# Kernel optimization log

Measured on AMD Instinct MI355X. Metric: run time of the kernel, lower is better.

Reference implementation:

```python
import jax, jax.numpy as jnp
import numpy as np

B, S, D, H = 1, 2048, 1024, 16
HD = D // H  # head_dim = 64


def _split_heads(x):
    # [B,S,D] -> [B,H,S,HD]
    return x.reshape(B, S, H, HD).transpose(0, 2, 1, 3)


def setup_inputs() -> dict:
    key = jax.random.key(0)
    ks = jax.random.split(key, 8)
    p = 0.02
    return {
        "hidden_states": jax.random.normal(ks[0], (B, S, D), jnp.float32),
        "knowledge": jax.random.normal(ks[1], (B, S, D), jnp.float32),
        "Wq": jax.random.normal(ks[2], (2 * D, D), jnp.float32) * p,
        "Wk_know": jax.random.normal(ks[3], (D, D), jnp.float32) * p,
        "Wk_mlp": jax.random.normal(ks[4], (D, D), jnp.float32) * p,
        "Wv_know": jax.random.normal(ks[5], (D, D), jnp.float32) * p,
        "Wv_mlp": jax.random.normal(ks[6], (D, D), jnp.float32) * p,
        "Wo": jax.random.normal(ks[7], (D, D), jnp.float32) * p,
    }


def reference(hidden_states, knowledge, Wq, Wk_know, Wk_mlp, Wv_know, Wv_mlp, Wo):
    shared = jnp.concatenate([hidden_states, knowledge], axis=-1)  # [B,S,2D]
    q = _split_heads(shared @ Wq)            # [B,H,S,HD]
    k_know = _split_heads(knowledge @ Wk_know)
    k_mlp = _split_heads(hidden_states @ Wk_mlp)
    v_know = _split_heads(knowledge @ Wv_know)
    v_mlp = _split_heads(hidden_states @ Wv_mlp)

    scale = jnp.asarray(D, jnp.float32) ** 0.5  # note: full embed_dim, not head_dim
    mask_value = jnp.finfo(jnp.float32).min
    causal = jnp.tril(jnp.ones((S, S), dtype=bool))  # [S,S]

    s_know = jnp.einsum("bhqd,bhkd->bhqk", q, k_know) / scale
    s_know = jnp.where(causal, s_know, mask_value)
    s_mlp = jnp.einsum("bhqd,bhkd->bhqk", q, k_mlp) / scale
    s_mlp = jnp.where(causal, s_mlp, mask_value)

    concat_scores = jax.nn.softmax(jnp.concatenate([s_know, s_mlp], axis=-1), axis=-1)  # [B,H,S,2S]
    concat_values = jnp.concatenate([v_know, v_mlp], axis=-2)  # [B,H,2S,HD]
    out = jnp.einsum("bhqk,bhkd->bhqd", concat_scores, concat_values)
    out = out.transpose(0, 2, 1, 3).reshape(B, S, D) @ Wo  # merge heads + proj_o
    return out, concat_scores
```

## Files before the change

### kernel.cpp

```cpp
#include <hip/hip_runtime.h>

typedef unsigned short u16;
typedef float f32x4 __attribute__((ext_vector_type(4)));
typedef __bf16 bf16x8 __attribute__((ext_vector_type(8)));
typedef unsigned int u32x4 __attribute__((ext_vector_type(4)));
typedef u16 u16x4 __attribute__((ext_vector_type(4)));

#define S_ 2048
#define D_ 1024
#define H_ 16
#define HD_ 64

#define WAITV(N) asm volatile("s_waitcnt vmcnt(" #N ")" ::: "memory")
#define BAR() __builtin_amdgcn_s_barrier()
#define SFENCE() __builtin_amdgcn_sched_barrier(0)

__device__ __forceinline__ u16 f2bf(float f) {
  unsigned int u = __builtin_bit_cast(unsigned int, f);
  u += 0x7fffu + ((u >> 16) & 1u);
  return (u16)(u >> 16);
}

__device__ __forceinline__ f32x4 mfma16(bf16x8 a, bf16x8 b, f32x4 c) {
  return __builtin_amdgcn_mfma_f32_16x16x32_bf16(a, b, c, 0, 0, 0);
}

__device__ __forceinline__ float ex2(float x) {
  float r;
  asm("v_exp_f32 %0, %1\n\ts_nop 1" : "=v"(r) : "v"(x));
  return r;
}

__device__ __forceinline__ void gld_lds16(const u16* g, u16* l) {
  __builtin_amdgcn_global_load_lds((const __attribute__((address_space(1))) void*)g,
                                   (__attribute__((address_space(3))) void*)l, 16, 0, 0);
}

__global__ __launch_bounds__(256) void prep_kernel(
    const float* __restrict__ hs, const float* __restrict__ kn, const float* __restrict__ Wq,
    const float* __restrict__ Wkk, const float* __restrict__ Wvk, const float* __restrict__ Wkm,
    const float* __restrict__ Wvm, const float* __restrict__ Wo, u16* __restrict__ hs_bf,
    u16* __restrict__ kn_bf, u16* __restrict__ WqT, u16* __restrict__ WkvkT,
    u16* __restrict__ WkvmT, u16* __restrict__ WoT, int n4) {
  __shared__ float tile[32][33];
  int b = blockIdx.x;
  if (b < 4096) {
    int i = b * 256 + threadIdx.x;
    const float* s;
    u16* d;
    int j;
    if (i < n4) { s = hs; d = hs_bf; j = i; }
    else { j = i - n4; if (j >= n4) return; s = kn; d = kn_bf; }
    f32x4 v = *(const f32x4*)(s + (size_t)j * 4);
    u16x4 o;
    o[0] = f2bf(v[0]); o[1] = f2bf(v[1]); o[2] = f2bf(v[2]); o[3] = f2bf(v[3]);
    *(u16x4*)(d + (size_t)j * 4) = o;
    return;
  }
  int idx = b - 4096;
  int bc = idx & 31, y = idx >> 5;
  const float* W;
  u16* WT;
  int R, br;
  const size_t HM = (size_t)1024 * 1024;
  if (y < 64) { W = Wq; WT = WqT; R = 2048; br = y; }
  else {
    R = 1024; br = y & 31;
    switch ((y - 64) >> 5) {
      case 0: W = Wkk; WT = WkvkT; break;
      case 1: W = Wvk; WT = WkvkT + HM; break;
      case 2: W = Wkm; WT = WkvmT; break;
      case 3: W = Wvm; WT = WkvmT + HM; break;
      default: W = Wo; WT = WoT; break;
    }
  }
  int tx = threadIdx.x & 31, ty = threadIdx.x >> 5;
#pragma unroll
  for (int i = 0; i < 4; ++i)
    tile[ty + i * 8][tx] = W[(size_t)(br * 32 + ty + i * 8) * 1024 + bc * 32 + tx];
  __syncthreads();
#pragma unroll
  for (int i = 0; i < 4; ++i)
    WT[(size_t)(bc * 32 + ty + i * 8) * R + br * 32 + tx] = f2bf(tile[tx][ty + i * 8]);
}

template <int MODE, int MI, int NI>
__device__ __forceinline__ void gemm_body(u16* smem, const u16* A0, const u16* A1, int ksplit,
                                          const u16* BT, void* Cp, int K, int ldc, int bn,
                                          int bm) {
  constexpr int BM = MI * 32, BN = NI * 32;
  u16* const As0 = smem;
  u16* const Bs0 = smem + 2 * BM * 32;
  const int tid = threadIdx.x, l = tid & 63, w = tid >> 6;
  const int wm = w >> 1, wn = w & 1;
  f32x4 zf = {0.f, 0.f, 0.f, 0.f};
  f32x4 acc[MI][NI];
#pragma unroll
  for (int mi = 0; mi < MI; ++mi)
#pragma unroll
    for (int ni = 0; ni < NI; ++ni) acc[mi][ni] = zf;

  auto STAGE = [&](int b, int t) {
    int k0 = t * 32;
#pragma unroll
    for (int i = 0; i < MI / 2; ++i) {
      int idx = tid + i * 256, r = idx >> 2, c = idx & 3;
      int sc = c ^ ((r >> 1) & 3);
      int k = k0 + sc * 8;
      const u16* src = (k < ksplit) ? (A0 + (size_t)(bm * BM + r) * D_ + k)
                                    : (A1 + (size_t)(bm * BM + r) * D_ + (k - ksplit));
      gld_lds16(src, As0 + b * BM * 32 + idx * 8);
    }
#pragma unroll
    for (int i = 0; i < NI / 2; ++i) {
      int idx = tid + i * 256, r = idx >> 2, c = idx & 3;
      int sc = c ^ ((r >> 1) & 3);
      gld_lds16(BT + (size_t)(bn * BN + r) * K + k0 + sc * 8, Bs0 + b * BN * 32 + idx * 8);
    }
  };

  const int nt = K >> 5;
  STAGE(0, 0);
  int cur = 0;
  for (int t = 0; t < nt; ++t) {
    if (t + 1 < nt) {
      STAGE(cur ^ 1, t + 1);
      if constexpr (MI + NI == 8) { WAITV(4); } else { WAITV(3); }
    } else {
      WAITV(0);
    }
    BAR(); SFENCE();
    const u16* Asc = As0 + cur * BM * 32;
    const u16* Bsc = Bs0 + cur * BN * 32;
    bf16x8 af[MI], bfr[NI];
#pragma unroll
    for (int mi = 0; mi < MI; ++mi) {
      int row = wm * (MI * 16) + mi * 16 + (l & 15);
      int slot = (l >> 4) ^ ((row >> 1) & 3);
      af[mi] = __builtin_bit_cast(bf16x8, *(const u32x4*)(Asc + row * 32 + slot * 8));
    }
#pragma unroll
    for (int ni = 0; ni < NI; ++ni) {
      int row = wn * (NI * 16) + ni * 16 + (l & 15);
      int slot = (l >> 4) ^ ((row >> 1) & 3);
      bfr[ni] = __builtin_bit_cast(bf16x8, *(const u32x4*)(Bsc + row * 32 + slot * 8));
    }
#pragma unroll
    for (int mi = 0; mi < MI; ++mi)
#pragma unroll
      for (int ni = 0; ni < NI; ++ni) acc[mi][ni] = mfma16(af[mi], bfr[ni], acc[mi][ni]);
    SFENCE(); BAR();
    cur ^= 1;
  }

  if constexpr (MODE == 2) {
#pragma unroll
    for (int mi = 0; mi < MI; ++mi)
#pragma unroll
      for (int ni = 0; ni < NI; ++ni) {
        u16x4 pk;
#pragma unroll
        for (int r = 0; r < 4; ++r) pk[r] = f2bf(acc[mi][ni][r]);
        int n = bn * BN + wn * (NI * 16) + ni * 16 + (l & 15);
        int m0 = bm * BM + wm * (MI * 16) + mi * 16 + (l >> 4) * 4;
        *(u16x4*)((u16*)Cp + (size_t)n * S_ + m0) = pk;
      }
  } else if constexpr (MODE == 0) {
    __syncthreads();
    u16* Cs = smem;
#pragma unroll
    for (int mi = 0; mi < MI; ++mi)
#pragma unroll
      for (int ni = 0; ni < NI; ++ni)
#pragma unroll
        for (int r = 0; r < 4; ++r) {
          int row = wm * (MI * 16) + mi * 16 + (l >> 4) * 4 + r;
          int col = wn * (NI * 16) + ni * 16 + (l & 15);
          Cs[row * 144 + col] = f2bf(acc[mi][ni][r]);
        }
    __syncthreads();
    constexpr int CPR = BN / 8;
#pragma unroll
    for (int i = 0; i < BM * CPR / 256; ++i) {
      int idx = tid + i * 256;
      int lr = idx / CPR, cc = idx % CPR;
      u32x4 v = *(const u32x4*)(Cs + lr * 144 + cc * 8);
      *(u32x4*)((u16*)Cp + (size_t)(bm * BM + lr) * ldc + bn * BN + cc * 8) = v;
    }
  } else {
    __syncthreads();
    float* Cs = (float*)smem;
#pragma unroll
    for (int mi = 0; mi < MI; ++mi)
#pragma unroll
      for (int ni = 0; ni < NI; ++ni)
#pragma unroll
        for (int r = 0; r < 4; ++r) {
          int row = wm * (MI * 16) + mi * 16 + (l >> 4) * 4 + r;
          int col = wn * (NI * 16) + ni * 16 + (l & 15);
          Cs[row * 136 + col] = acc[mi][ni][r];
        }
    __syncthreads();
    constexpr int CPR = BN / 4;
#pragma unroll
    for (int i = 0; i < BM * CPR / 256; ++i) {
      int idx = tid + i * 256;
      int lr = idx / CPR, cc = idx % CPR;
      f32x4 v = *(const f32x4*)(Cs + lr * 136 + cc * 4);
      __builtin_nontemporal_store(v, (f32x4*)((float*)Cp + (size_t)(bm * BM + lr) * ldc +
                                              bn * BN + cc * 4));
    }
  }
}

__global__ __launch_bounds__(256) void proj_gemm(const u16* __restrict__ hs_bf,
                                                 const u16* __restrict__ kn_bf,
                                                 const u16* __restrict__ WqT,
                                                 const u16* __restrict__ WkvkT,
                                                 const u16* __restrict__ WkvmT,
                                                 u16* __restrict__ qb, u16* __restrict__ kk,
                                                 u16* __restrict__ km, u16* __restrict__ vkT,
                                                 u16* __restrict__ vmT) {
  __shared__ __attribute__((aligned(16))) u16 smem[18432];
  int bid = blockIdx.x;
  int xcd = bid & 7, ixd = bid >> 3;
  int bm, bn;
  if (ixd < 16) {
    bm = xcd * 2 + (ixd >> 3);
    bn = ixd & 7;
  } else if (ixd >= 64 && ixd < 80) {
    return;
  } else {
    int s = (ixd < 64) ? (ixd - 16) : (48 + (ixd - 80));
    bm = xcd * 2 + (s >> 5);
    bn = 8 + (s & 31);
  }
  const size_t HM = (size_t)1024 * 1024;
  const int BIG = 1 << 30;
  if (bn < 8) {
    gemm_body<0, 4, 4>(smem, hs_bf, kn_bf, 1024, WqT, qb, 2048, 1024, bn, bm);
  } else if (bn < 16) {
    gemm_body<0, 4, 4>(smem, kn_bf, kn_bf, BIG, WkvkT, kk, 1024, 1024, bn - 8, bm);
  } else if (bn < 24) {
    gemm_body<2, 4, 4>(smem, kn_bf, kn_bf, BIG, WkvkT + HM, vkT, 1024, 0, bn - 16, bm);
  } else if (bn < 32) {
    gemm_body<0, 4, 4>(smem, hs_bf, hs_bf, BIG, WkvmT, km, 1024, 1024, bn - 24, bm);
  } else {
    gemm_body<2, 4, 4>(smem, hs_bf, hs_bf, BIG, WkvmT + HM, vmT, 1024, 0, bn - 32, bm);
  }
}

__global__ __launch_bounds__(256) void out_gemm(const u16* __restrict__ aob,
                                                const u16* __restrict__ WoT,
                                                float* __restrict__ out) {
  __shared__ __attribute__((aligned(16))) u16 smem[17408];
  int bid = blockIdx.x;
  int xcd = bid & 7, i = bid >> 3;
  int bm = xcd * 4 + (i >> 3), bn = i & 7;
  gemm_body<1, 2, 4>(smem, aob, aob, 1 << 30, WoT, out, 1024, 1024, bn, bm);
}

__device__ __forceinline__ void stage_async64_t256(u16* dst, const u16* src, int stride,
                                                   int tid) {
#pragma unroll
  for (int j = 0; j < 2; ++j) {
    int ci = tid + j * 256;
    int r = ci >> 3, c = ci & 7;
    int sc = c ^ (r & 7);
    gld_lds16(src + (size_t)r * stride + sc * 8, dst + ci * 8);
  }
}

__device__ __forceinline__ bf16x8 ld_frag64(const u16* lds, int rowbase, int chunkbase, int l) {
  int row = rowbase + (l & 15);
  int chunk = chunkbase + (l >> 4);
  int slot = chunk ^ (row & 7);
  return __builtin_bit_cast(bf16x8, *(const u32x4*)(lds + row * 64 + slot * 8));
}

__global__ __launch_bounds__(256) void attn_kernel(const u16* __restrict__ qb,
                                                   const u16* __restrict__ kk,
                                                   const u16* __restrict__ km,
                                                   const u16* __restrict__ vkT,
                                                   const u16* __restrict__ vmT,
                                                   float* __restrict__ scores,
                                                   u16* __restrict__ ao) {
  const int fid = blockIdx.x;
  const int xcd = fid & 7, ixd = fid >> 3;
  const int h = xcd * 2 + (ixd >> 5);
  const int j = ixd & 31;
  const int a = j >> 1;
  const int qt = (((j & 1) ^ (ixd >> 5)) == 0) ? (31 - a) : a;
  const int tid = threadIdx.x, w = tid >> 6, l = tid & 63;
  const int nt = qt + 1;
  const int NT = 2 * nt;
  const int qrow0 = qt * 64;
  const int q16 = l & 15, c4 = l >> 4;
  const int qme = qrow0 + w * 16 + q16;
  const float sc2 = 0.04508422f;

  __shared__ u16 qs[64 * 64];
  __shared__ u16 kv4[4][64 * 64];
  __shared__ u16 ps[64 * 64];

  auto kptr = [&](int it) {
    int hf = it >= nt;
    int t = it - (hf ? nt : 0);
    const u16* kb = hf ? km : kk;
    return kb + (size_t)(t * 64) * 1024 + h * HD_;
  };
  auto vptr = [&](int it) {
    int hf = it >= nt;
    int t = it - (hf ? nt : 0);
    const u16* vb = hf ? vmT : vkT;
    return vb + (size_t)(h * HD_) * S_ + t * 64;
  };

#pragma unroll
  for (int i = 0; i < 2; ++i) {
    int idx = tid + i * 256;
    int r = idx >> 3, c = idx & 7;
    u32x4 v = *(const u32x4*)(qb + (size_t)(qrow0 + r) * D_ + h * HD_ + c * 8);
    *(u32x4*)(qs + r * 64 + ((c ^ (r & 7)) * 8)) = v;
  }
  __syncthreads();
  bf16x8 qA0 = ld_frag64(qs, w * 16, 0, l);
  bf16x8 qA1 = ld_frag64(qs, w * 16, 4, l);

  float aa[4] = {0.f, 0.f, 0.f, 0.f};
  stage_async64_t256(kv4[0], kptr(0), 1024, tid);
  stage_async64_t256(kv4[1], kptr(1), 1024, tid);
  for (int p = 0; p < NT; p += 2) {
    WAITV(0);
    BAR(); SFENCE();
    int base = ((p >> 1) & 1) ? 2 : 0;
    if (p + 2 < NT) {
      int nb = base ^ 2;
      stage_async64_t256(kv4[nb], kptr(p + 2), 1024, tid);
      stage_async64_t256(kv4[nb + 1], kptr(p + 3), 1024, tid);
    }
    __builtin_amdgcn_s_setprio(1);
#pragma unroll
    for (int half = 0; half < 2; ++half) {
      int it = p + half;
      const u16* ksb = kv4[base + half];
      int domask = (it == nt - 1) || (it == NT - 1);
      int tbase = (it - (it >= nt ? nt : 0)) * 64;
      f32x4 zfv = {0.f, 0.f, 0.f, 0.f};
#pragma unroll
      for (int kf = 0; kf < 4; ++kf) {
        f32x4 z = zfv;
        z = mfma16(ld_frag64(ksb, kf * 16, 0, l), qA0, z);
        z = mfma16(ld_frag64(ksb, kf * 16, 4, l), qA1, z);
#pragma unroll
        for (int r = 0; r < 4; ++r) {
          float v = z[r];
          if (domask) {
            int key = tbase + kf * 16 + c4 * 4 + r;
            if (key > qme) v = -1e30f;
          }
          aa[r] += ex2(v * sc2);
        }
      }
    }
    __builtin_amdgcn_s_setprio(0);
    SFENCE();
  }
  BAR();
  float psum = (aa[0] + aa[1]) + (aa[2] + aa[3]);
  psum += __shfl_xor(psum, 16, 64);
  psum += __shfl_xor(psum, 32, 64);
  const float moff = __log2f(psum);

  f32x4 zf = {0.f, 0.f, 0.f, 0.f};
  f32x4 o[4];
#pragma unroll
  for (int df = 0; df < 4; ++df) o[df] = zf;

  float* const srow0 = scores + ((size_t)h * S_ + qme) * (2 * S_) + c4 * 4;
  const int prow = w * 16 + q16;
  const int swz8 = (q16 & 7) << 1;

  stage_async64_t256(kv4[0], kptr(0), 1024, tid);
  stage_async64_t256(kv4[2], vptr(0), S_, tid);
  int cur = 0;
  for (int it = 0; it < NT; ++it) {
    if (it == 0) { WAITV(0); } else { WAITV(4); }
    BAR(); SFENCE();
    if (it + 1 < NT) {
      stage_async64_t256(kv4[cur ^ 1], kptr(it + 1), 1024, tid);
      stage_async64_t256(kv4[2 + (cur ^ 1)], vptr(it + 1), S_, tid);
    }
    int domask = (it == nt - 1) || (it == NT - 1);
    int hf = it >= nt;
    int tbase = (it - (hf ? nt : 0)) * 64;
    float pv[16];
    __builtin_amdgcn_s_setprio(1);
#pragma unroll
    for (int kf = 0; kf < 4; ++kf) {
      f32x4 z = zf;
      z = mfma16(ld_frag64(kv4[cur], kf * 16, 0, l), qA0, z);
      z = mfma16(ld_frag64(kv4[cur], kf * 16, 4, l), qA1, z);
#pragma unroll
      for (int r = 0; r < 4; ++r) {
        float v = z[r];
        if (domask) {
          int key = tbase + kf * 16 + c4 * 4 + r;
          if (key > qme) v = -1e30f;
        }
        pv[kf * 4 + r] = ex2(__builtin_fmaf(v, sc2, -moff));
      }
    }
    __builtin_amdgcn_s_setprio(0);
    float* srow = srow0 + hf * S_ + tbase;
#pragma unroll
    for (int kf = 0; kf < 4; ++kf) {
      f32x4 s4 = {pv[kf * 4], pv[kf * 4 + 1], pv[kf * 4 + 2], pv[kf * 4 + 3]};
      *(f32x4*)(srow + kf * 16) = s4;
    }
#pragma unroll
    for (int kf = 0; kf < 4; ++kf) {
      u16x4 pk;
#pragma unroll
      for (int r = 0; r < 4; ++r) pk[r] = f2bf(pv[kf * 4 + r]);
      int slot8 = (kf * 4 + c4) ^ swz8;
      *(u16x4*)(ps + prow * 64 + slot8 * 4) = pk;
    }
    __builtin_amdgcn_s_setprio(1);
#pragma unroll
    for (int df = 0; df < 4; ++df)
#pragma unroll
      for (int kc = 0; kc < 2; ++kc)
        o[df] = mfma16(ld_frag64(kv4[2 + cur], df * 16, kc * 4, l),
                       ld_frag64(ps, w * 16, kc * 4, l), o[df]);
    __builtin_amdgcn_s_setprio(0);
    SFENCE();
    cur ^= 1;
  }
#pragma unroll
  for (int df = 0; df < 4; ++df) {
    u16x4 pk;
#pragma unroll
    for (int r = 0; r < 4; ++r) pk[r] = f2bf(o[df][r]);
    *(u16x4*)(ao + (size_t)qme * D_ + h * HD_ + df * 16 + c4 * 4) = pk;
  }

  int zc = 2048 - nt * 64;
  if (zc > 0) {
    int vph = zc >> 2;
    f32x4 zero = {0.f, 0.f, 0.f, 0.f};
    float* base = scores + ((size_t)h * S_ + qrow0) * (2 * S_) + nt * 64;
    for (int row = 0; row < 64; ++row) {
      float* rp = base + (size_t)row * (2 * S_);
      for (int i = tid; i < vph; i += 256)
        __builtin_nontemporal_store(zero, (f32x4*)(rp + i * 4));
      for (int i = tid; i < vph; i += 256)
        __builtin_nontemporal_store(zero, (f32x4*)(rp + S_ + i * 4));
    }
  }
}

extern "C" void kernel_launch(void* const* d_in, const int* in_sizes, int n_in, void* d_out,
                              int out_size, void* d_ws, size_t ws_size, hipStream_t stream) {
  const float* hs = (const float*)d_in[0];
  const float* kn = (const float*)d_in[1];
  const float* Wq = (const float*)d_in[2];
  const float* Wkk = (const float*)d_in[3];
  const float* Wkm = (const float*)d_in[4];
  const float* Wvk = (const float*)d_in[5];
  const float* Wvm = (const float*)d_in[6];
  const float* Wo = (const float*)d_in[7];
  float* out = (float*)d_out;
  float* scores = out + (size_t)S_ * D_;

  const size_t M2 = (size_t)S_ * D_;
  u16* ws = (u16*)d_ws;
  u16* hs_bf = ws;
  u16* kn_bf = hs_bf + M2;
  u16* WqT = kn_bf + M2;
  u16* WkvkT = WqT + M2;
  u16* WkvmT = WkvkT + M2;
  u16* WoT = WkvmT + M2;
  u16* qb = WoT + M2 / 2;
  u16* kk = qb + M2;
  u16* km = kk + M2;
  u16* vkT = km + M2;
  u16* vmT = vkT + M2;
  u16* aob = vmT + M2;

  int n4 = (int)(M2 / 4);
  prep_kernel<<<11264, 256, 0, stream>>>(hs, kn, Wq, Wkk, Wvk, Wkm, Wvm, Wo, hs_bf, kn_bf, WqT,
                                         WkvkT, WkvmT, WoT, n4);
  proj_gemm<<<768, 256, 0, stream>>>(hs_bf, kn_bf, WqT, WkvkT, WkvmT, qb, kk, km, vkT, vmT);
  attn_kernel<<<512, 256, 0, stream>>>(qb, kk, km, vkT, vmT, scores, aob);
  out_gemm<<<256, 256, 0, stream>>>(aob, WoT, out);
}
```

Before: 200.9 us.

## Split attention key dimension across two wave groups with 512-thread blocks

Doubles the attention block to 512 threads. Each group of four waves handles half of each 64-key tile for both the softmax-sum pass and the P·V pass. Partial row sums are merged through shared memory, and the partial output accumulators are reduced through LDS before the bf16 store. The aim is more waves per block to hide latency and spread the score writes, in exchange for extra barriers and an LDS reduction step.

```diff
diff --git a/kernel.cpp b/kernel.cpp
--- a/kernel.cpp
+++ b/kernel.cpp
@@ -260,15 +260,12 @@
   gemm_body<1, 2, 4>(smem, aob, aob, 1 << 30, WoT, out, 1024, 1024, bn, bm);
 }
 
-__device__ __forceinline__ void stage_async64_t256(u16* dst, const u16* src, int stride,
+__device__ __forceinline__ void stage_async64_t512(u16* dst, const u16* src, int stride,
                                                    int tid) {
-#pragma unroll
-  for (int j = 0; j < 2; ++j) {
-    int ci = tid + j * 256;
-    int r = ci >> 3, c = ci & 7;
-    int sc = c ^ (r & 7);
-    gld_lds16(src + (size_t)r * stride + sc * 8, dst + ci * 8);
-  }
+  int ci = tid;
+  int r = ci >> 3, c = ci & 7;
+  int sc = c ^ (r & 7);
+  gld_lds16(src + (size_t)r * stride + sc * 8, dst + ci * 8);
 }
 
 __device__ __forceinline__ bf16x8 ld_frag64(const u16* lds, int rowbase, int chunkbase, int l) {
@@ -278,7 +275,7 @@
   return __builtin_bit_cast(bf16x8, *(const u32x4*)(lds + row * 64 + slot * 8));
 }
 
-__global__ __launch_bounds__(256) void attn_kernel(const u16* __restrict__ qb,
+__global__ __launch_bounds__(512) void attn_kernel(const u16* __restrict__ qb,
                                                    const u16* __restrict__ kk,
                                                    const u16* __restrict__ km,
                                                    const u16* __restrict__ vkT,
@@ -292,16 +289,18 @@
   const int a = j >> 1;
   const int qt = (((j & 1) ^ (ixd >> 5)) == 0) ? (31 - a) : a;
   const int tid = threadIdx.x, w = tid >> 6, l = tid & 63;
+  const int wk = w & 3, kh = w >> 2;
   const int nt = qt + 1;
   const int NT = 2 * nt;
   const int qrow0 = qt * 64;
   const int q16 = l & 15, c4 = l >> 4;
-  const int qme = qrow0 + w * 16 + q16;
+  const int qme = qrow0 + wk * 16 + q16;
   const float sc2 = 0.04508422f;
 
   __shared__ u16 qs[64 * 64];
   __shared__ u16 kv4[4][64 * 64];
   __shared__ u16 ps[64 * 64];
+  __shared__ float stat[128];
 
   auto kptr = [&](int it) {
     int hf = it >= nt;
@@ -316,28 +315,26 @@
     return vb + (size_t)(h * HD_) * S_ + t * 64;
   };
 
-#pragma unroll
-  for (int i = 0; i < 2; ++i) {
-    int idx = tid + i * 256;
-    int r = idx >> 3, c = idx & 7;
+  {
+    int r = tid >> 3, c = tid & 7;
     u32x4 v = *(const u32x4*)(qb + (size_t)(qrow0 + r) * D_ + h * HD_ + c * 8);
     *(u32x4*)(qs + r * 64 + ((c ^ (r & 7)) * 8)) = v;
   }
   __syncthreads();
-  bf16x8 qA0 = ld_frag64(qs, w * 16, 0, l);
-  bf16x8 qA1 = ld_frag64(qs, w * 16, 4, l);
+  bf16x8 qA0 = ld_frag64(qs, wk * 16, 0, l);
+  bf16x8 qA1 = ld_frag64(qs, wk * 16, 4, l);
 
   float aa[4] = {0.f, 0.f, 0.f, 0.f};
-  stage_async64_t256(kv4[0], kptr(0), 1024, tid);
-  stage_async64_t256(kv4[1], kptr(1), 1024, tid);
+  stage_async64_t512(kv4[0], kptr(0), 1024, tid);
+  stage_async64_t512(kv4[1], kptr(1), 1024, tid);
   for (int p = 0; p < NT; p += 2) {
     WAITV(0);
     BAR(); SFENCE();
     int base = ((p >> 1) & 1) ? 2 : 0;
     if (p + 2 < NT) {
       int nb = base ^ 2;
-      stage_async64_t256(kv4[nb], kptr(p + 2), 1024, tid);
-      stage_async64_t256(kv4[nb + 1], kptr(p + 3), 1024, tid);
+      stage_async64_t512(kv4[nb], kptr(p + 2), 1024, tid);
+      stage_async64_t512(kv4[nb + 1], kptr(p + 3), 1024, tid);
     }
     __builtin_amdgcn_s_setprio(1);
 #pragma unroll
@@ -348,7 +345,8 @@
       int tbase = (it - (it >= nt ? nt : 0)) * 64;
       f32x4 zfv = {0.f, 0.f, 0.f, 0.f};
 #pragma unroll
-      for (int kf = 0; kf < 4; ++kf) {
+      for (int jf = 0; jf < 2; ++jf) {
+        int kf = kh * 2 + jf;
         f32x4 z = zfv;
         z = mfma16(ld_frag64(ksb, kf * 16, 0, l), qA0, z);
         z = mfma16(ld_frag64(ksb, kf * 16, 4, l), qA1, z);
@@ -366,11 +364,13 @@
     __builtin_amdgcn_s_setprio(0);
     SFENCE();
   }
-  BAR();
   float psum = (aa[0] + aa[1]) + (aa[2] + aa[3]);
   psum += __shfl_xor(psum, 16, 64);
   psum += __shfl_xor(psum, 32, 64);
-  const float moff = __log2f(psum);
+  if (l < 16) stat[w * 16 + l] = psum;
+  __syncthreads();
+  const float lsum = stat[wk * 16 + q16] + stat[(wk + 4) * 16 + q16];
+  const float moff = __log2f(lsum);
 
   f32x4 zf = {0.f, 0.f, 0.f, 0.f};
   f32x4 o[4];
@@ -378,26 +378,27 @@
   for (int df = 0; df < 4; ++df) o[df] = zf;
 
   float* const srow0 = scores + ((size_t)h * S_ + qme) * (2 * S_) + c4 * 4;
-  const int prow = w * 16 + q16;
+  const int prow = wk * 16 + q16;
   const int swz8 = (q16 & 7) << 1;
 
-  stage_async64_t256(kv4[0], kptr(0), 1024, tid);
-  stage_async64_t256(kv4[2], vptr(0), S_, tid);
+  stage_async64_t512(kv4[0], kptr(0), 1024, tid);
+  stage_async64_t512(kv4[2], vptr(0), S_, tid);
   int cur = 0;
   for (int it = 0; it < NT; ++it) {
-    if (it == 0) { WAITV(0); } else { WAITV(4); }
+    if (it == 0) { WAITV(0); } else { WAITV(2); }
     BAR(); SFENCE();
     if (it + 1 < NT) {
-      stage_async64_t256(kv4[cur ^ 1], kptr(it + 1), 1024, tid);
-      stage_async64_t256(kv4[2 + (cur ^ 1)], vptr(it + 1), S_, tid);
+      stage_async64_t512(kv4[cur ^ 1], kptr(it + 1), 1024, tid);
+      stage_async64_t512(kv4[2 + (cur ^ 1)], vptr(it + 1), S_, tid);
     }
     int domask = (it == nt - 1) || (it == NT - 1);
     int hf = it >= nt;
     int tbase = (it - (hf ? nt : 0)) * 64;
-    float pv[16];
+    float pv[8];
     __builtin_amdgcn_s_setprio(1);
 #pragma unroll
-    for (int kf = 0; kf < 4; ++kf) {
+    for (int jf = 0; jf < 2; ++jf) {
+      int kf = kh * 2 + jf;
       f32x4 z = zf;
       z = mfma16(ld_frag64(kv4[cur], kf * 16, 0, l), qA0, z);
       z = mfma16(ld_frag64(kv4[cur], kf * 16, 4, l), qA1, z);
@@ -408,41 +409,59 @@
           int key = tbase + kf * 16 + c4 * 4 + r;
           if (key > qme) v = -1e30f;
         }
-        pv[kf * 4 + r] = ex2(__builtin_fmaf(v, sc2, -moff));
+        pv[jf * 4 + r] = ex2(__builtin_fmaf(v, sc2, -moff));
       }
     }
     __builtin_amdgcn_s_setprio(0);
     float* srow = srow0 + hf * S_ + tbase;
 #pragma unroll
-    for (int kf = 0; kf < 4; ++kf) {
-      f32x4 s4 = {pv[kf * 4], pv[kf * 4 + 1], pv[kf * 4 + 2], pv[kf * 4 + 3]};
+    for (int jf = 0; jf < 2; ++jf) {
+      int kf = kh * 2 + jf;
+      f32x4 s4 = {pv[jf * 4], pv[jf * 4 + 1], pv[jf * 4 + 2], pv[jf * 4 + 3]};
       *(f32x4*)(srow + kf * 16) = s4;
     }
 #pragma unroll
-    for (int kf = 0; kf < 4; ++kf) {
+    for (int jf = 0; jf < 2; ++jf) {
+      int kf = kh * 2 + jf;
       u16x4 pk;
 #pragma unroll
-      for (int r = 0; r < 4; ++r) pk[r] = f2bf(pv[kf * 4 + r]);
+      for (int r = 0; r < 4; ++r) pk[r] = f2bf(pv[jf * 4 + r]);
       int slot8 = (kf * 4 + c4) ^ swz8;
       *(u16x4*)(ps + prow * 64 + slot8 * 4) = pk;
     }
     __builtin_amdgcn_s_setprio(1);
-#pragma unroll
-    for (int df = 0; df < 4; ++df)
-#pragma unroll
-      for (int kc = 0; kc < 2; ++kc)
-        o[df] = mfma16(ld_frag64(kv4[2 + cur], df * 16, kc * 4, l),
-                       ld_frag64(ps, w * 16, kc * 4, l), o[df]);
+    {
+      bf16x8 pa = ld_frag64(ps, wk * 16, kh * 4, l);
+#pragma unroll
+      for (int df = 0; df < 4; ++df)
+        o[df] = mfma16(ld_frag64(kv4[2 + cur], df * 16, kh * 4, l), pa, o[df]);
+    }
     __builtin_amdgcn_s_setprio(0);
     SFENCE();
     cur ^= 1;
   }
-#pragma unroll
-  for (int df = 0; df < 4; ++df) {
-    u16x4 pk;
-#pragma unroll
-    for (int r = 0; r < 4; ++r) pk[r] = f2bf(o[df][r]);
-    *(u16x4*)(ao + (size_t)qme * D_ + h * HD_ + df * 16 + c4 * 4) = pk;
+
+  __syncthreads();
+  float* obuf = (float*)kv4;
+  if (kh == 1) {
+#pragma unroll
+    for (int df = 0; df < 4; ++df)
+#pragma unroll
+      for (int r = 0; r < 4; ++r)
+        obuf[((wk * 4 + df) * 16 + c4 * 4 + r) * 16 + q16] = o[df][r];
+  }
+  __syncthreads();
+  if (kh == 0) {
+#pragma unroll
+    for (int df = 0; df < 4; ++df) {
+      u16x4 pk;
+#pragma unroll
+      for (int r = 0; r < 4; ++r) {
+        float t = o[df][r] + obuf[((wk * 4 + df) * 16 + c4 * 4 + r) * 16 + q16];
+        pk[r] = f2bf(t);
+      }
+      *(u16x4*)(ao + (size_t)qme * D_ + h * HD_ + df * 16 + c4 * 4) = pk;
+    }
   }
 
   int zc = 2048 - nt * 64;
@@ -452,9 +471,9 @@
     float* base = scores + ((size_t)h * S_ + qrow0) * (2 * S_) + nt * 64;
     for (int row = 0; row < 64; ++row) {
       float* rp = base + (size_t)row * (2 * S_);
-      for (int i = tid; i < vph; i += 256)
+      for (int i = tid; i < vph; i += 512)
         __builtin_nontemporal_store(zero, (f32x4*)(rp + i * 4));
-      for (int i = tid; i < vph; i += 256)
+      for (int i = tid; i < vph; i += 512)
         __builtin_nontemporal_store(zero, (f32x4*)(rp + S_ + i * 4));
     }
   }
@@ -492,6 +511,6 @@
   prep_kernel<<<11264, 256, 0, stream>>>(hs, kn, Wq, Wkk, Wvk, Wkm, Wvm, Wo, hs_bf, kn_bf, WqT,
                                          WkvkT, WkvmT, WoT, n4);
   proj_gemm<<<768, 256, 0, stream>>>(hs_bf, kn_bf, WqT, WkvkT, WkvmT, qb, kk, km, vkT, vmT);
-  attn_kernel<<<512, 256, 0, stream>>>(qb, kk, km, vkT, vmT, scores, aob);
+  attn_kernel<<<512, 512, 0, stream>>>(qb, kk, km, vkT, vmT, scores, aob);
   out_gemm<<<256, 256, 0, stream>>>(aob, WoT, out);
 }
```

New measurement: 191.3 us. 4.8% less time.
